# Kernel tuning notes

Measured on AMD Instinct MI355X. Metric: run time of the kernel, lower is better.

## Reference

```python
import jax, jax.numpy as jnp
import numpy as np

B, T, D = 8, 4096, 1024
N_EXPERTS, N_SLOTS = 64, 8
HID = 256


def setup_inputs() -> dict:
    key = jax.random.key(0)
    ks = jax.random.split(key, 8)
    s = lambda *sh: 1.0 / np.sqrt(sh[-2]) if len(sh) >= 2 else 0.02
    tokens = jax.random.normal(ks[0], (B, T, D), dtype=jnp.float32)
    # routing weights, original uses np.random.random -> uniform [0,1); scale down for stability
    expert_mixture = jax.random.uniform(ks[1], (D, N_EXPERTS * N_SLOTS), dtype=jnp.float32) * 0.02
    W1 = jax.random.normal(ks[2], (N_EXPERTS, D, HID), dtype=jnp.float32) / np.sqrt(D)
    b1 = jnp.zeros((N_EXPERTS, HID), dtype=jnp.float32)
    W2 = jax.random.normal(ks[3], (N_EXPERTS, HID, HID), dtype=jnp.float32) / np.sqrt(HID)
    b2 = jnp.zeros((N_EXPERTS, HID), dtype=jnp.float32)
    W3 = jax.random.normal(ks[4], (N_EXPERTS, HID, D), dtype=jnp.float32) / np.sqrt(HID)
    b3 = jnp.zeros((N_EXPERTS, D), dtype=jnp.float32)
    return {"tokens": tokens, "expert_mixture": expert_mixture,
            "W1": W1, "b1": b1, "W2": W2, "b2": b2, "W3": W3, "b3": b3}


def reference(tokens, expert_mixture, W1, b1, W2, b2, W3, b3):
    b, t, d = tokens.shape
    flat = tokens.reshape(-1, d)                       # [BT, D]
    mat = flat @ expert_mixture                        # [BT, n*p]
    row_probs = jax.nn.softmax(mat, axis=0)            # over tokens
    col_probs = jax.nn.softmax(mat, axis=1)            # over slots
    x_hat = row_probs.T @ flat                         # [n*p, D] dispatch
    xs = x_hat.reshape(N_EXPERTS, N_SLOTS, d)          # [n, p, D]
    # per-expert MLP: Linear-ReLU-Linear-ReLU-Linear (batched over experts)
    h = jax.nn.relu(jnp.einsum('npd,ndh->nph', xs, W1) + b1[:, None, :])
    h = jax.nn.relu(jnp.einsum('nph,nhk->npk', h, W2) + b2[:, None, :])
    y_hat = jnp.einsum('npk,nkd->npd', h, W3) + b3[:, None, :]
    y_hat = y_hat.reshape(N_EXPERTS * N_SLOTS, d)      # [n*p, D]
    y = col_probs @ y_hat                              # [BT, D] combine
    return y.reshape(b, t, d)
```

## Files before the change

### kernel.cpp

```cpp
#include <hip/hip_runtime.h>
#include <math.h>

namespace {

constexpr int BT  = 8 * 4096;
constexpr int DIM = 1024;
constexpr int NE  = 64;
constexpr int NS  = 8;
constexpr int NP  = NE * NS;
constexpr int HID = 256;

typedef float f32x4 __attribute__((ext_vector_type(4)));
typedef __bf16 bf16x8 __attribute__((ext_vector_type(8)));
typedef short s16x8 __attribute__((ext_vector_type(8)));

__device__ __forceinline__ ushort f2bf(float x) {
  union { float f; unsigned u; } a; a.f = x;
  unsigned r = a.u + 0x7FFFu + ((a.u >> 16) & 1u);
  return (ushort)(r >> 16);
}
__device__ __forceinline__ float bf2f(ushort u) {
  union { unsigned u; float f; } a; a.u = (unsigned)u << 16;
  return a.f;
}

__device__ __forceinline__ void gload16(const void* g, void* l) {
  __builtin_amdgcn_global_load_lds(
      (const __attribute__((address_space(1))) void*)g,
      (__attribute__((address_space(3))) void*)l, 16, 0, 0);
}

template <bool ATOMIC, bool OBF, bool CSTAT>
__global__ __launch_bounds__(512) void k_gemm(const ushort* __restrict__ A,
                                              const ushort* __restrict__ Bt,
                                              void* __restrict__ Cv,
                                              int N, int kchunk,
                                              int lda, int ldb,
                                              float* __restrict__ pmOut,
                                              float* __restrict__ pzOut) {
  __shared__ __align__(16) ushort As0[256 * 64];
  __shared__ __align__(16) ushort As1[256 * 64];
  __shared__ __align__(16) ushort As2[256 * 64];
  __shared__ __align__(16) ushort Bs0[128 * 64];
  __shared__ __align__(16) ushort Bs1[128 * 64];
  __shared__ __align__(16) ushort Bs2[128 * 64];

  const int tid = threadIdx.x;
  const int wid = tid >> 6;
  const int lane = tid & 63;

  const int gx = gridDim.x, gy = gridDim.y;
  int wg = (blockIdx.z * gy + blockIdx.y) * gx + blockIdx.x;
  const int nwg = gx * gy * gridDim.z;
  wg = (wg & 7) * (nwg >> 3) + (wg >> 3);
  const int bx = wg % gx;
  const int rest = wg / gx;
  const int by = rest % gy;
  const int bz = rest / gy;

  const int n0 = bx * 128;
  const int m0 = by * 256;
  const int kb = bz * kchunk;

  const int w8 = wid * 8;
  const int lr = lane >> 3;
  const int ks = (((lane & 7) ^ lr) * 8);
  const ushort* Asrc = A + (size_t)(m0 + w8 + lr) * lda + ks;
  const ushort* Bsrc = Bt + (size_t)(n0 + w8 + lr) * ldb + ks;

  const int wm64 = (wid >> 1) * 64;
  const int wn64 = (wid & 1) * 64;
  const int fr = lane & 15;
  const int fq = lane >> 4;
  const int fq8 = fq * 8;
  const int frsw = (fr & 7) << 3;

  f32x4 acc[4][4];
#pragma unroll
  for (int i = 0; i < 4; ++i)
#pragma unroll
    for (int j = 0; j < 4; ++j) acc[i][j] = (f32x4){0.f, 0.f, 0.f, 0.f};

  const int nt = kchunk / 64;

#define STAGE6(An_, Bn_, kt_)                                                    \
  do {                                                                           \
    _Pragma("unroll") for (int q = 0; q < 4; ++q)                                \
      gload16(Asrc + (size_t)(q * 64) * lda + (kt_), (An_) + (q * 64 + w8) * 64);\
    _Pragma("unroll") for (int q = 0; q < 2; ++q)                                \
      gload16(Bsrc + (size_t)(q * 64) * ldb + (kt_), (Bn_) + (q * 64 + w8) * 64);\
  } while (0)

#define LD(B_, r_, h_)                                                          \
  __builtin_bit_cast(bf16x8, *(const s16x8*)((B_) + (size_t)(r_) * 64 +         \
                                             (((h_) * 32 + fq8) ^ frsw)))

#define GBLOCK(Ab_, Bb_, An_, Bn_, tt_)                                         \
  do {                                                                          \
    if ((tt_) + 1 < nt) asm volatile("s_waitcnt vmcnt(6)" ::: "memory");        \
    else                asm volatile("s_waitcnt vmcnt(0)" ::: "memory");        \
    __builtin_amdgcn_sched_barrier(0);                                          \
    __builtin_amdgcn_s_barrier();                                               \
    __builtin_amdgcn_sched_barrier(0);                                          \
    if ((tt_) + 2 < nt) STAGE6(An_, Bn_, kb + ((tt_) + 2) * 64);                \
    bf16x8 bfr_[4][2];                                                          \
    _Pragma("unroll") for (int n = 0; n < 4; ++n) {                             \
      bfr_[n][0] = LD(Bb_, wn64 + n * 16 + fr, 0);                              \
      bfr_[n][1] = LD(Bb_, wn64 + n * 16 + fr, 1);                              \
    }                                                                           \
    _Pragma("unroll") for (int m = 0; m < 4; ++m) {                             \
      bf16x8 a0_ = LD(Ab_, wm64 + m * 16 + fr, 0);                              \
      bf16x8 a1_ = LD(Ab_, wm64 + m * 16 + fr, 1);                              \
      __builtin_amdgcn_s_setprio(1);                                            \
      _Pragma("unroll") for (int n = 0; n < 4; ++n)                             \
        acc[m][n] = __builtin_amdgcn_mfma_f32_16x16x32_bf16(a0_, bfr_[n][0],    \
                                                            acc[m][n], 0, 0, 0);\
      _Pragma("unroll") for (int n = 0; n < 4; ++n)                             \
        acc[m][n] = __builtin_amdgcn_mfma_f32_16x16x32_bf16(a1_, bfr_[n][1],    \
                                                            acc[m][n], 0, 0, 0);\
      __builtin_amdgcn_s_setprio(0);                                            \
    }                                                                           \
  } while (0)

  STAGE6(As0, Bs0, kb);
  STAGE6(As1, Bs1, kb + 64);
  int t = 0;
  for (; t + 3 <= nt; t += 3) {
    GBLOCK(As0, Bs0, As2, Bs2, t);
    GBLOCK(As1, Bs1, As0, Bs0, t + 1);
    GBLOCK(As2, Bs2, As1, Bs1, t + 2);
  }
  if (t < nt) { GBLOCK(As0, Bs0, As2, Bs2, t); ++t; }
  if (t < nt) { GBLOCK(As1, Bs1, As0, Bs0, t); ++t; }
#undef GBLOCK
#undef LD
#undef STAGE6

  if (OBF) {
    ushort* Cb = (ushort*)Cv + (size_t)(m0 + wm64 + fq * 4) * N + n0 + wn64 + fr;
#pragma unroll
    for (int m = 0; m < 4; ++m)
#pragma unroll
      for (int n = 0; n < 4; ++n)
#pragma unroll
        for (int r = 0; r < 4; ++r)
          Cb[(size_t)(m * 16 + r) * N + n * 16] = f2bf(acc[m][n][r]);
  } else {
    float* Cb = (float*)Cv + (size_t)(m0 + wm64 + fq * 4) * N + n0 + wn64 + fr;
#pragma unroll
    for (int m = 0; m < 4; ++m)
#pragma unroll
      for (int n = 0; n < 4; ++n)
#pragma unroll
        for (int r = 0; r < 4; ++r) {
          float* p = Cb + (size_t)(m * 16 + r) * N + n * 16;
          if (ATOMIC) atomicAdd(p, acc[m][n][r]);
          else *p = acc[m][n][r];
        }
  }

  if (CSTAT) {
    float cm_[4], cz_[4];
#pragma unroll
    for (int n = 0; n < 4; ++n) { cm_[n] = -INFINITY; cz_[n] = 0.f; }
#pragma unroll
    for (int m = 0; m < 4; ++m)
#pragma unroll
      for (int n = 0; n < 4; ++n)
#pragma unroll
        for (int r = 0; r < 4; ++r) {
          float v = acc[m][n][r];
          float mm = fmaxf(cm_[n], v);
          cz_[n] = cz_[n] * __expf(cm_[n] - mm) + __expf(v - mm);
          cm_[n] = mm;
        }
#pragma unroll
    for (int off = 16; off <= 32; off <<= 1)
#pragma unroll
      for (int n = 0; n < 4; ++n) {
        float m2 = __shfl_xor(cm_[n], off);
        float z2 = __shfl_xor(cz_[n], off);
        float mm = fmaxf(cm_[n], m2);
        cz_[n] = cz_[n] * __expf(cm_[n] - mm) + z2 * __expf(m2 - mm);
        cm_[n] = mm;
      }
    __syncthreads();
    float* smx = (float*)As0;
    float* smz = smx + 4 * 128;
    const int mrow = wid >> 1;
    if (lane < 16) {
#pragma unroll
      for (int n = 0; n < 4; ++n) {
        smx[mrow * 128 + wn64 + n * 16 + lane] = cm_[n];
        smz[mrow * 128 + wn64 + n * 16 + lane] = cz_[n];
      }
    }
    __syncthreads();
    if (tid < 128) {
      float m = smx[tid], z = smz[tid];
#pragma unroll
      for (int p = 1; p < 4; ++p) {
        float m2 = smx[p * 128 + tid], z2 = smz[p * 128 + tid];
        float mm = fmaxf(m, m2);
        z = z * __expf(m - mm) + z2 * __expf(m2 - mm);
        m = mm;
      }
      pmOut[(size_t)by * NP + n0 + tid] = m;
      pzOut[(size_t)by * NP + n0 + tid] = z;
    }
  }
}

__global__ __launch_bounds__(256) void k_convert(const float* __restrict__ X,
                                                 ushort* __restrict__ Y,
                                                 size_t n) {
  size_t i = ((size_t)blockIdx.x * 256 + threadIdx.x) * 8;
  const size_t stride = (size_t)gridDim.x * 256 * 8;
  for (; i < n; i += stride) {
    float4 a = *(const float4*)(X + i);
    float4 b = *(const float4*)(X + i + 4);
    s16x8 o;
    o[0] = (short)f2bf(a.x); o[1] = (short)f2bf(a.y);
    o[2] = (short)f2bf(a.z); o[3] = (short)f2bf(a.w);
    o[4] = (short)f2bf(b.x); o[5] = (short)f2bf(b.y);
    o[6] = (short)f2bf(b.z); o[7] = (short)f2bf(b.w);
    *(s16x8*)(Y + i) = o;
  }
}

__global__ __launch_bounds__(256) void k_tpose(const ushort* __restrict__ X,
                                               ushort* __restrict__ Yt,
                                               int Cc, int ldt) {
  __shared__ __align__(16) ushort tT[64][256];
  const int tid = threadIdx.x;
  const int r0 = blockIdx.x * 256, c0 = blockIdx.y * 64;
#pragma unroll
  for (int i = 0; i < 8; ++i) {
    const int idx = i * 256 + tid;
    const int r = idx >> 3, c8 = (idx & 7) * 8;
    s16x8 v = *(const s16x8*)(X + (size_t)(r0 + r) * Cc + c0 + c8);
#pragma unroll
    for (int j = 0; j < 8; ++j)
      tT[c8 + j][r ^ (((c8 + j) & 7) << 3)] = (ushort)v[j];
  }
  __syncthreads();
#pragma unroll
  for (int i = 0; i < 8; ++i) {
    const int idx = i * 256 + tid;
    const int c = idx >> 5, r8 = (idx & 31) * 8;
    s16x8 o = *(const s16x8*)&tT[c][r8 ^ ((c & 7) << 3)];
    *(s16x8*)(Yt + (size_t)(c0 + c) * ldt + r0 + r8) = o;
  }
}

template <bool ROWM, bool TRANSP>
__global__ __launch_bounds__(256) void k_cvt(const float* __restrict__ X,
                                             ushort* __restrict__ Yrm,
                                             ushort* __restrict__ Yt,
                                             int Cc, int ldt) {
  __shared__ __align__(16) ushort tT[64][256];
  const int tid = threadIdx.x;
  const int r0 = blockIdx.x * 256, c0 = blockIdx.y * 64;
#pragma unroll
  for (int i = 0; i < 16; ++i) {
    const int idx = i * 256 + tid;
    const int r = idx >> 4, c4 = (idx & 15) * 4;
    float4 v = *(const float4*)(X + (size_t)(r0 + r) * Cc + c0 + c4);
    ushort u[4] = {f2bf(v.x), f2bf(v.y), f2bf(v.z), f2bf(v.w)};
    if (ROWM) {
      ushort4 o = make_ushort4(u[0], u[1], u[2], u[3]);
      *(ushort4*)(Yrm + (size_t)(r0 + r) * Cc + c0 + c4) = o;
    }
    if (TRANSP) {
#pragma unroll
      for (int j = 0; j < 4; ++j)
        tT[c4 + j][r ^ (((c4 + j) & 7) << 3)] = u[j];
    }
  }
  if (TRANSP) {
    __syncthreads();
#pragma unroll
    for (int i = 0; i < 8; ++i) {
      const int idx = i * 256 + tid;
      const int c = idx >> 5, r8 = (idx & 31) * 8;
      s16x8 o = *(const s16x8*)&tT[c][r8 ^ ((c & 7) << 3)];
      *(s16x8*)(Yt + (size_t)(c0 + c) * ldt + r0 + r8) = o;
    }
  }
}

__global__ __launch_bounds__(256) void k_colfinal(const float* __restrict__ pm,
                                                  const float* __restrict__ pz,
                                                  float* __restrict__ colM,
                                                  float* __restrict__ colIZ) {
  const int col = blockIdx.x * 64 + (threadIdx.x & 63);
  const int q = threadIdx.x >> 6;
  float m = -INFINITY, z = 0.f;
  for (int r = q; r < BT / 256; r += 4) {
    float m2 = pm[(size_t)r * NP + col], z2 = pz[(size_t)r * NP + col];
    float mm = fmaxf(m, m2);
    z = z * __expf(m - mm) + z2 * __expf(m2 - mm);
    m = mm;
  }
  __shared__ float sm[4][64], sz[4][64];
  sm[q][threadIdx.x & 63] = m;
  sz[q][threadIdx.x & 63] = z;
  __syncthreads();
  if (q == 0) {
    for (int p = 1; p < 4; ++p) {
      float m2 = sm[p][threadIdx.x], z2 = sz[p][threadIdx.x];
      float mm = fmaxf(m, m2);
      z = z * __expf(m - mm) + z2 * __expf(m2 - mm);
      m = mm;
    }
    colM[col] = m;
    colIZ[col] = 1.f / z;
  }
}

__global__ __launch_bounds__(256) void k_rowstats(const ushort* __restrict__ mat,
                                                  float* __restrict__ rowM,
                                                  float* __restrict__ rowIZ) {
  const int w = threadIdx.x >> 6;
  const int lane = threadIdx.x & 63;
  const int t = blockIdx.x * 4 + w;
  s16x8 v = *(const s16x8*)(mat + (size_t)t * NP + lane * 8);
  float f[8];
#pragma unroll
  for (int j = 0; j < 8; ++j) f[j] = bf2f((ushort)v[j]);
  float m = f[0];
#pragma unroll
  for (int j = 1; j < 8; ++j) m = fmaxf(m, f[j]);
#pragma unroll
  for (int o = 32; o; o >>= 1) m = fmaxf(m, __shfl_xor(m, o));
  float s = 0.f;
#pragma unroll
  for (int j = 0; j < 8; ++j) s += __expf(f[j] - m);
#pragma unroll
  for (int o = 32; o; o >>= 1) s += __shfl_xor(s, o);
  if (lane == 0) {
    rowM[t] = m;
    rowIZ[t] = 1.f / s;
  }
}

__global__ __launch_bounds__(256) void k_probs(const ushort* __restrict__ mat,
                                               const float* __restrict__ colM,
                                               const float* __restrict__ colIZ,
                                               const float* __restrict__ rowM,
                                               const float* __restrict__ rowIZ,
                                               ushort* __restrict__ Pc,
                                               ushort* __restrict__ Pt) {
  __shared__ __align__(16) ushort tT[64][256];
  __shared__ float cm[64], cz[64], rm[256], rz[256];
  const int tid = threadIdx.x;
  const int t0 = blockIdx.x * 256, s0 = blockIdx.y * 64;
  if (tid < 64) {
    cm[tid] = colM[s0 + tid];
    cz[tid] = colIZ[s0 + tid];
  }
  rm[tid] = rowM[t0 + tid];
  rz[tid] = rowIZ[t0 + tid];
  __syncthreads();
#pragma unroll
  for (int i = 0; i < 8; ++i) {
    const int idx = i * 256 + tid;
    const int r = idx >> 3, c8 = (idx & 7) * 8;
    s16x8 v = *(const s16x8*)(mat + (size_t)(t0 + r) * NP + s0 + c8);
    const float mr = rm[r], zr = rz[r];
    s16x8 oc;
#pragma unroll
    for (int j = 0; j < 8; ++j) {
      float f = bf2f((ushort)v[j]);
      oc[j] = (short)f2bf(__expf(f - mr) * zr);
      tT[c8 + j][r ^ (((c8 + j) & 7) << 3)] = f2bf(__expf(f - cm[c8 + j]) * cz[c8 + j]);
    }
    *(s16x8*)(Pc + (size_t)(t0 + r) * NP + s0 + c8) = oc;
  }
  __syncthreads();
#pragma unroll
  for (int i = 0; i < 8; ++i) {
    const int idx = i * 256 + tid;
    const int c = idx >> 5, r8 = (idx & 31) * 8;
    s16x8 o = *(const s16x8*)&tT[c][r8 ^ ((c & 7) << 3)];
    *(s16x8*)(Pt + (size_t)(s0 + c) * BT + t0 + r8) = o;
  }
}

template <int K, int N, bool RELU>
__global__ __launch_bounds__(256) void k_mlp(const float* __restrict__ X,
                                             const float* __restrict__ W,
                                             const float* __restrict__ bias,
                                             float* __restrict__ Y) {
  __shared__ float xs[NS * K];
  const int tid = threadIdx.x;
  const int e = blockIdx.x;
  const float4* src = (const float4*)(X + (size_t)e * NS * K);
  float4* dst = (float4*)xs;
  constexpr int NV = (NS * K) / (4 * 256);
#pragma unroll
  for (int i = 0; i < NV; ++i) dst[tid + i * 256] = src[tid + i * 256];
  __syncthreads();
  const int j = blockIdx.y * 64 + (tid & 63);
  const int pr = tid >> 6;
  const float* w = W + (size_t)e * K * N + j;
  const float* x0 = xs + pr * K;
  const float* x1 = xs + (pr + 4) * K;
  float a0 = 0.f, a1 = 0.f;
#pragma unroll 8
  for (int k = 0; k < K; ++k) {
    float wv = w[(size_t)k * N];
    a0 += x0[k] * wv;
    a1 += x1[k] * wv;
  }
  const float bb = bias[(size_t)e * N + j];
  a0 += bb;
  a1 += bb;
  if (RELU) {
    a0 = fmaxf(a0, 0.f);
    a1 = fmaxf(a1, 0.f);
  }
  Y[((size_t)e * NS + pr) * N + j] = a0;
  Y[((size_t)e * NS + pr + 4) * N + j] = a1;
}

}

extern "C" void kernel_launch(void* const* d_in, const int* in_sizes, int n_in,
                              void* d_out, int out_size, void* d_ws, size_t ws_size,
                              hipStream_t stream) {
  const float* tokens = (const float*)d_in[0];
  const float* em     = (const float*)d_in[1];
  const float* W1     = (const float*)d_in[2];
  const float* b1     = (const float*)d_in[3];
  const float* W2     = (const float*)d_in[4];
  const float* b2     = (const float*)d_in[5];
  const float* W3     = (const float*)d_in[6];
  const float* b3     = (const float*)d_in[7];
  float* out = (float*)d_out;

  char* w = (char*)d_ws;
  ushort* matb      = (ushort*)w; w += (size_t)BT * NP * 2;
  ushort* tokens_bf = (ushort*)w; w += (size_t)BT * DIM * 2;
  ushort* tokT      = (ushort*)w; w += (size_t)DIM * BT * 2;
  ushort* Pt        = (ushort*)w; w += (size_t)NP * BT * 2;
  ushort* Pc        = (ushort*)w; w += (size_t)BT * NP * 2;
  ushort* emT       = (ushort*)w; w += (size_t)NP * DIM * 2;
  ushort* yhatT     = (ushort*)w; w += (size_t)DIM * NP * 2;
  float*  pm        = (float*)w;  w += (size_t)(BT / 256) * NP * 4;
  float*  pz        = (float*)w;  w += (size_t)(BT / 256) * NP * 4;
  float*  colM      = (float*)w;  w += NP * 4;
  float*  colIZ     = (float*)w;  w += NP * 4;
  float*  rowM      = (float*)w;  w += BT * 4;
  float*  rowIZ     = (float*)w;  w += BT * 4;
  float*  xhat      = (float*)w;  w += (size_t)NP * DIM * 4;
  float*  h1        = (float*)w;  w += (size_t)NP * HID * 4;
  float*  h2        = (float*)w;  w += (size_t)NP * HID * 4;
  float*  yhat      = (float*)w;  w += (size_t)NP * DIM * 4;
  (void)ws_size; (void)in_sizes; (void)n_in; (void)out_size;

  k_convert<<<2048, 256, 0, stream>>>(tokens, tokens_bf, (size_t)BT * DIM);
  k_tpose<<<dim3(BT / 256, DIM / 64), 256, 0, stream>>>(tokens_bf, tokT, DIM, BT);
  k_cvt<false, true><<<dim3(DIM / 256, NP / 64), 256, 0, stream>>>(em, nullptr, emT, NP, DIM);
  k_gemm<false, true, true><<<dim3(NP / 128, BT / 256, 1), 512, 0, stream>>>(
      tokens_bf, emT, matb, NP, DIM, DIM, DIM, pm, pz);
  k_colfinal<<<NP / 64, 256, 0, stream>>>(pm, pz, colM, colIZ);
  k_rowstats<<<BT / 4, 256, 0, stream>>>(matb, rowM, rowIZ);
  k_probs<<<dim3(BT / 256, NP / 64), 256, 0, stream>>>(matb, colM, colIZ, rowM, rowIZ, Pc, Pt);
  hipMemsetAsync(xhat, 0, (size_t)NP * DIM * 4, stream);
  k_gemm<true, false, false><<<dim3(DIM / 128, NP / 256, 16), 512, 0, stream>>>(
      Pt, tokT, xhat, DIM, BT / 16, BT, BT, nullptr, nullptr);
  k_mlp<DIM, HID, true><<<dim3(NE, HID / 64), 256, 0, stream>>>(xhat, W1, b1, h1);
  k_mlp<HID, HID, true><<<dim3(NE, HID / 64), 256, 0, stream>>>(h1, W2, b2, h2);
  k_mlp<HID, DIM, false><<<dim3(NE, DIM / 64), 256, 0, stream>>>(h2, W3, b3, yhat);
  k_cvt<false, true><<<dim3(NP / 256, DIM / 64), 256, 0, stream>>>(yhat, nullptr, yhatT, DIM, NP);
  k_gemm<false, false, false><<<dim3(DIM / 128, BT / 256, 1), 512, 0, stream>>>(
      Pc, yhatT, out, DIM, NP, NP, NP, nullptr, nullptr);
}
```

Baseline: 388.6 us.

## Fuse row-softmax stats into routing GEMM epilogue and split-K the expert MLPs

Per-row max and sum-exp partials are now computed in the routing GEMM epilogue and written per column-block. A small finalize kernel merges the four partials, replacing the separate row-stats pass that re-read the bf16 logits matrix. The expert MLP kernels are split along K with atomicAdd accumulation into bias-initialised outputs. ReLU moves to the input load of the next layer, which raises the block count for these low-parallelism kernels. The cost is three extra bias-init launches, float atomics with nondeterministic summation order, and more epilogue work and register pressure in the GEMM.

```diff
diff --git a/kernel.cpp b/kernel.cpp
--- a/kernel.cpp
+++ b/kernel.cpp
@@ -37,7 +37,9 @@
                                               int N, int kchunk,
                                               int lda, int ldb,
                                               float* __restrict__ pmOut,
-                                              float* __restrict__ pzOut) {
+                                              float* __restrict__ pzOut,
+                                              float* __restrict__ rpmOut,
+                                              float* __restrict__ rpzOut) {
   __shared__ __align__(16) ushort As0[256 * 64];
   __shared__ __align__(16) ushort As1[256 * 64];
   __shared__ __align__(16) ushort As2[256 * 64];
@@ -184,9 +186,33 @@
         cz_[n] = cz_[n] * __expf(cm_[n] - mm) + z2 * __expf(m2 - mm);
         cm_[n] = mm;
       }
+    float rm_[16], rz_[16];
+#pragma unroll
+    for (int m = 0; m < 4; ++m)
+#pragma unroll
+      for (int r = 0; r < 4; ++r) {
+        const int i = m * 4 + r;
+        float mx = fmaxf(fmaxf(acc[m][0][r], acc[m][1][r]),
+                         fmaxf(acc[m][2][r], acc[m][3][r]));
+        rm_[i] = mx;
+        rz_[i] = __expf(acc[m][0][r] - mx) + __expf(acc[m][1][r] - mx) +
+                 __expf(acc[m][2][r] - mx) + __expf(acc[m][3][r] - mx);
+      }
+#pragma unroll
+    for (int off = 1; off <= 8; off <<= 1)
+#pragma unroll
+      for (int i = 0; i < 16; ++i) {
+        float m2 = __shfl_xor(rm_[i], off);
+        float z2 = __shfl_xor(rz_[i], off);
+        float mm = fmaxf(rm_[i], m2);
+        rz_[i] = rz_[i] * __expf(rm_[i] - mm) + z2 * __expf(m2 - mm);
+        rm_[i] = mm;
+      }
     __syncthreads();
     float* smx = (float*)As0;
     float* smz = smx + 4 * 128;
+    float* smr = (float*)Bs0;
+    float* smz2 = smr + 512;
     const int mrow = wid >> 1;
     if (lane < 16) {
 #pragma unroll
@@ -194,6 +220,16 @@
         smx[mrow * 128 + wn64 + n * 16 + lane] = cm_[n];
         smz[mrow * 128 + wn64 + n * 16 + lane] = cz_[n];
       }
+    }
+    if (fr == 0) {
+#pragma unroll
+      for (int m = 0; m < 4; ++m)
+#pragma unroll
+        for (int r = 0; r < 4; ++r) {
+          const int row = wm64 + m * 16 + fq * 4 + r;
+          smr[(wid & 1) * 256 + row] = rm_[m * 4 + r];
+          smz2[(wid & 1) * 256 + row] = rz_[m * 4 + r];
+        }
     }
     __syncthreads();
     if (tid < 128) {
@@ -207,6 +243,14 @@
       }
       pmOut[(size_t)by * NP + n0 + tid] = m;
       pzOut[(size_t)by * NP + n0 + tid] = z;
+    }
+    if (tid < 256) {
+      float m1 = smr[tid], z1 = smz2[tid];
+      float m2 = smr[256 + tid], z2 = smz2[256 + tid];
+      float mm = fmaxf(m1, m2);
+      float zz = z1 * __expf(m1 - mm) + z2 * __expf(m2 - mm);
+      rpmOut[(size_t)bx * BT + m0 + tid] = mm;
+      rpzOut[(size_t)bx * BT + m0 + tid] = zz;
     }
   }
 }
@@ -318,30 +362,21 @@
   }
 }
 
-__global__ __launch_bounds__(256) void k_rowstats(const ushort* __restrict__ mat,
+__global__ __launch_bounds__(256) void k_rowfinal(const float* __restrict__ rpm,
+                                                  const float* __restrict__ rpz,
                                                   float* __restrict__ rowM,
                                                   float* __restrict__ rowIZ) {
-  const int w = threadIdx.x >> 6;
-  const int lane = threadIdx.x & 63;
-  const int t = blockIdx.x * 4 + w;
-  s16x8 v = *(const s16x8*)(mat + (size_t)t * NP + lane * 8);
-  float f[8];
-#pragma unroll
-  for (int j = 0; j < 8; ++j) f[j] = bf2f((ushort)v[j]);
-  float m = f[0];
-#pragma unroll
-  for (int j = 1; j < 8; ++j) m = fmaxf(m, f[j]);
-#pragma unroll
-  for (int o = 32; o; o >>= 1) m = fmaxf(m, __shfl_xor(m, o));
-  float s = 0.f;
-#pragma unroll
-  for (int j = 0; j < 8; ++j) s += __expf(f[j] - m);
-#pragma unroll
-  for (int o = 32; o; o >>= 1) s += __shfl_xor(s, o);
-  if (lane == 0) {
-    rowM[t] = m;
-    rowIZ[t] = 1.f / s;
-  }
+  const int t = blockIdx.x * 256 + threadIdx.x;
+  float m = -INFINITY, z = 0.f;
+#pragma unroll
+  for (int c = 0; c < 4; ++c) {
+    float m2 = rpm[(size_t)c * BT + t], z2 = rpz[(size_t)c * BT + t];
+    float mm = fmaxf(m, m2);
+    z = z * __expf(m - mm) + z2 * __expf(m2 - mm);
+    m = mm;
+  }
+  rowM[t] = m;
+  rowIZ[t] = 1.f / z;
 }
 
 __global__ __launch_bounds__(256) void k_probs(const ushort* __restrict__ mat,
@@ -387,41 +422,49 @@
   }
 }
 
-template <int K, int N, bool RELU>
+__global__ __launch_bounds__(256) void k_binit(const float* __restrict__ bias,
+                                               float* __restrict__ Y, int N) {
+  const int idx = blockIdx.x * 256 + threadIdx.x;
+  const int ep = idx / N, j = idx % N;
+  Y[idx] = bias[(size_t)(ep / NS) * N + j];
+}
+
+template <int K, int N, int KS, bool RELU_IN>
 __global__ __launch_bounds__(256) void k_mlp(const float* __restrict__ X,
                                              const float* __restrict__ W,
-                                             const float* __restrict__ bias,
                                              float* __restrict__ Y) {
-  __shared__ float xs[NS * K];
+  constexpr int KSL = K / KS;
+  __shared__ float xs[NS * KSL];
   const int tid = threadIdx.x;
   const int e = blockIdx.x;
-  const float4* src = (const float4*)(X + (size_t)e * NS * K);
-  float4* dst = (float4*)xs;
-  constexpr int NV = (NS * K) / (4 * 256);
-#pragma unroll
-  for (int i = 0; i < NV; ++i) dst[tid + i * 256] = src[tid + i * 256];
+  const int k0 = blockIdx.z * KSL;
+  constexpr int NV = (NS * KSL) / (4 * 256);
+#pragma unroll
+  for (int i = 0; i < NV; ++i) {
+    const int i4 = i * 256 + tid;
+    const int p = i4 / (KSL / 4), kk4 = (i4 % (KSL / 4)) * 4;
+    float4 v = *(const float4*)(X + (size_t)(e * NS + p) * K + k0 + kk4);
+    if (RELU_IN) {
+      v.x = fmaxf(v.x, 0.f); v.y = fmaxf(v.y, 0.f);
+      v.z = fmaxf(v.z, 0.f); v.w = fmaxf(v.w, 0.f);
+    }
+    *(float4*)(xs + p * KSL + kk4) = v;
+  }
   __syncthreads();
   const int j = blockIdx.y * 64 + (tid & 63);
   const int pr = tid >> 6;
-  const float* w = W + (size_t)e * K * N + j;
-  const float* x0 = xs + pr * K;
-  const float* x1 = xs + (pr + 4) * K;
+  const float* w = W + (size_t)e * K * N + (size_t)k0 * N + j;
+  const float* x0 = xs + pr * KSL;
+  const float* x1 = xs + (pr + 4) * KSL;
   float a0 = 0.f, a1 = 0.f;
 #pragma unroll 8
-  for (int k = 0; k < K; ++k) {
+  for (int k = 0; k < KSL; ++k) {
     float wv = w[(size_t)k * N];
     a0 += x0[k] * wv;
     a1 += x1[k] * wv;
   }
-  const float bb = bias[(size_t)e * N + j];
-  a0 += bb;
-  a1 += bb;
-  if (RELU) {
-    a0 = fmaxf(a0, 0.f);
-    a1 = fmaxf(a1, 0.f);
-  }
-  Y[((size_t)e * NS + pr) * N + j] = a0;
-  Y[((size_t)e * NS + pr + 4) * N + j] = a1;
+  atomicAdd(Y + (size_t)(e * NS + pr) * N + j, a0);
+  atomicAdd(Y + (size_t)(e * NS + pr + 4) * N + j, a1);
 }
 
 }
@@ -449,6 +492,8 @@
   ushort* yhatT     = (ushort*)w; w += (size_t)DIM * NP * 2;
   float*  pm        = (float*)w;  w += (size_t)(BT / 256) * NP * 4;
   float*  pz        = (float*)w;  w += (size_t)(BT / 256) * NP * 4;
+  float*  rpm       = (float*)w;  w += (size_t)4 * BT * 4;
+  float*  rpz       = (float*)w;  w += (size_t)4 * BT * 4;
   float*  colM      = (float*)w;  w += NP * 4;
   float*  colIZ     = (float*)w;  w += NP * 4;
   float*  rowM      = (float*)w;  w += BT * 4;
@@ -463,17 +508,20 @@
   k_tpose<<<dim3(BT / 256, DIM / 64), 256, 0, stream>>>(tokens_bf, tokT, DIM, BT);
   k_cvt<false, true><<<dim3(DIM / 256, NP / 64), 256, 0, stream>>>(em, nullptr, emT, NP, DIM);
   k_gemm<false, true, true><<<dim3(NP / 128, BT / 256, 1), 512, 0, stream>>>(
-      tokens_bf, emT, matb, NP, DIM, DIM, DIM, pm, pz);
+      tokens_bf, emT, matb, NP, DIM, DIM, DIM, pm, pz, rpm, rpz);
   k_colfinal<<<NP / 64, 256, 0, stream>>>(pm, pz, colM, colIZ);
-  k_rowstats<<<BT / 4, 256, 0, stream>>>(matb, rowM, rowIZ);
+  k_rowfinal<<<BT / 256, 256, 0, stream>>>(rpm, rpz, rowM, rowIZ);
   k_probs<<<dim3(BT / 256, NP / 64), 256, 0, stream>>>(matb, colM, colIZ, rowM, rowIZ, Pc, Pt);
   hipMemsetAsync(xhat, 0, (size_t)NP * DIM * 4, stream);
   k_gemm<true, false, false><<<dim3(DIM / 128, NP / 256, 16), 512, 0, stream>>>(
-      Pt, tokT, xhat, DIM, BT / 16, BT, BT, nullptr, nullptr);
-  k_mlp<DIM, HID, true><<<dim3(NE, HID / 64), 256, 0, stream>>>(xhat, W1, b1, h1);
-  k_mlp<HID, HID, true><<<dim3(NE, HID / 64), 256, 0, stream>>>(h1, W2, b2, h2);
-  k_mlp<HID, DIM, false><<<dim3(NE, DIM / 64), 256, 0, stream>>>(h2, W3, b3, yhat);
+      Pt, tokT, xhat, DIM, BT / 16, BT, BT, nullptr, nullptr, nullptr, nullptr);
+  k_binit<<<(NP * HID) / 256, 256, 0, stream>>>(b1, h1, HID);
+  k_binit<<<(NP * HID) / 256, 256, 0, stream>>>(b2, h2, HID);
+  k_binit<<<(NP * DIM) / 256, 256, 0, stream>>>(b3, yhat, DIM);
+  k_mlp<DIM, HID, 4, false><<<dim3(NE, HID / 64, 4), 256, 0, stream>>>(xhat, W1, h1);
+  k_mlp<HID, HID, 2, true><<<dim3(NE, HID / 64, 2), 256, 0, stream>>>(h1, W2, h2);
+  k_mlp<HID, DIM, 2, true><<<dim3(NE, DIM / 64, 2), 256, 0, stream>>>(h2, W3, yhat);
   k_cvt<false, true><<<dim3(NP / 256, DIM / 64), 256, 0, stream>>>(yhat, nullptr, yhatT, DIM, NP);
   k_gemm<false, false, false><<<dim3(DIM / 128, BT / 256, 1), 512, 0, stream>>>(
-      Pc, yhatT, out, DIM, NP, NP, NP, nullptr, nullptr);
-}
+      Pc, yhatT, out, DIM, NP, NP, NP, nullptr, nullptr, nullptr, nullptr);
+}
```

Measured after the change: 344.3 us. -11.4%, faster.
